# Performance work log

Hardware: AMD Instinct MI355X
Metric: run time of the kernel (lower is better)

Reference implementation:

```python
import jax, jax.numpy as jnp
import numpy as np

B, T, C, H, DFF = 4, 1024, 1024, 16, 4096
HS = C // H  # 64
EPS = 1e-5


def layer_norm(x, g, b):
    mu = jnp.mean(x, axis=-1, keepdims=True)
    var = jnp.var(x, axis=-1, keepdims=True)
    return (x - mu) * jax.lax.rsqrt(var + EPS) * g + b


def setup_inputs() -> dict:
    key = jax.random.key(0)
    ks = jax.random.split(key, 12)
    s = 0.02
    return {
        "x": jax.random.normal(ks[0], (B, T, C), jnp.float32),
        "wq": jax.random.normal(ks[1], (H, C, HS), jnp.float32) * s,
        "wk": jax.random.normal(ks[2], (H, C, HS), jnp.float32) * s,
        "wv": jax.random.normal(ks[3], (H, C, HS), jnp.float32) * s,
        "w_proj": jax.random.normal(ks[4], (H * HS, C), jnp.float32) * s,
        "b_proj": jnp.zeros((C,), jnp.float32),
        "w1": jax.random.normal(ks[5], (C, DFF), jnp.float32) * s,
        "b1": jnp.zeros((DFF,), jnp.float32),
        "w2": jax.random.normal(ks[6], (DFF, C), jnp.float32) * s,
        "b2": jnp.zeros((C,), jnp.float32),
        "g1": jnp.ones((C,), jnp.float32),
        "be1": jnp.zeros((C,), jnp.float32),
        "g2": jnp.ones((C,), jnp.float32),
        "be2": jnp.zeros((C,), jnp.float32),
    }


def reference(x, wq, wk, wv, w_proj, b_proj, w1, b1, w2, b2, g1, be1, g2, be2):
    h = layer_norm(x, g1, be1)
    # per-head projections, vectorized over heads: [B,H,T,HS]
    q = jnp.einsum('btc,hcd->bhtd', h, wq)
    k = jnp.einsum('btc,hcd->bhtd', h, wk)
    v = jnp.einsum('btc,hcd->bhtd', h, wv)
    # mask=None in the original forward, so no causal masking
    wei = jnp.einsum('bhtd,bhsd->bhts', q, k) * (HS ** -0.5)
    wei = jax.nn.softmax(wei, axis=-1)  # [B,H,T,T]
    out = jnp.einsum('bhts,bhsd->bhtd', wei, v)
    out = out.transpose(0, 2, 1, 3).reshape(B, T, H * HS)  # concat heads
    attn_out = out @ w_proj + b_proj
    x = x + attn_out
    h2 = layer_norm(x, g2, be2)
    ff = jax.nn.relu(h2 @ w1 + b1) @ w2 + b2
    x = x + ff
    return x, wei
```

## Files before the change

kernel.cpp:

```cpp
#include <hip/hip_runtime.h>
#include <hip/hip_bf16.h>

#define BB    4
#define TT    1024
#define CC    1024
#define HH    16
#define HSZ   64
#define DFF   4096
#define NTOK  (BB*TT)
#define BHN   (BB*HH)

typedef __attribute__((ext_vector_type(8))) short bf16x8;
typedef __attribute__((ext_vector_type(4))) float f32x4;

__device__ __forceinline__ ushort f2b(float v) {
    union { float f; unsigned u; } c; c.f = v;
    unsigned r = c.u + 0x7fffu + ((c.u >> 16) & 1u);
    return (ushort)(r >> 16);
}
__device__ __forceinline__ void stv(float* p, float v)  { *p = v; }
__device__ __forceinline__ void stv(ushort* p, float v) { *p = f2b(v); }

__device__ __forceinline__ void gload16(const void* g, void* l) {
    __builtin_amdgcn_global_load_lds(
        (const __attribute__((address_space(1))) void*)g,
        (__attribute__((address_space(3))) void*)l, 16, 0, 0);
}

__global__ __launch_bounds__(256)
void ln_k(const float* __restrict__ x, const float* __restrict__ g,
          const float* __restrict__ be, ushort* __restrict__ o)
{
    __shared__ float s1[4], s2[4];
    long row = blockIdx.x;
    const float4* xr = (const float4*)(x + row * CC);
    float4 v = xr[threadIdx.x];
    float a = v.x + v.y + v.z + v.w;
    float b = v.x*v.x + v.y*v.y + v.z*v.z + v.w*v.w;
    for (int off = 32; off > 0; off >>= 1) {
        a += __shfl_down(a, off);
        b += __shfl_down(b, off);
    }
    if ((threadIdx.x & 63) == 0) { s1[threadIdx.x >> 6] = a; s2[threadIdx.x >> 6] = b; }
    __syncthreads();
    float sum = s1[0] + s1[1] + s1[2] + s1[3];
    float sq  = s2[0] + s2[1] + s2[2] + s2[3];
    float mu  = sum * (1.0f / CC);
    float var = sq * (1.0f / CC) - mu * mu;
    float inv = rsqrtf(var + 1e-5f);
    float4 gg = ((const float4*)g)[threadIdx.x];
    float4 bb = ((const float4*)be)[threadIdx.x];
    ushort4 r;
    r.x = f2b((v.x - mu) * inv * gg.x + bb.x);
    r.y = f2b((v.y - mu) * inv * gg.y + bb.y);
    r.z = f2b((v.z - mu) * inv * gg.z + bb.z);
    r.w = f2b((v.w - mu) * inv * gg.w + bb.w);
    ((ushort4*)(o + row * CC))[threadIdx.x] = r;
}

__global__ __launch_bounds__(256)
void cvtall_k(const float* __restrict__ wq, const float* __restrict__ wk,
              const float* __restrict__ wv, const float* __restrict__ wproj,
              const float* __restrict__ w1, const float* __restrict__ w2,
              ushort* __restrict__ wqkvT, ushort* __restrict__ wpT,
              ushort* __restrict__ w1T, ushort* __restrict__ w2T)
{
    __shared__ float t[32][33];
    int idx = blockIdx.x;
    const float* src; ushort* dst; int R, Cc, bx, by;
    if (idx < 3072) {
        int seg = idx >> 10, rem = idx & 1023;
        int z = rem >> 6, tt2 = rem & 63;
        src = (seg == 0 ? wq : seg == 1 ? wk : wv) + (long)z * 65536;
        dst = wqkvT + (long)seg * (1L << 20) + (long)z * 65536;
        R = 1024; Cc = 64; bx = tt2 & 1; by = tt2 >> 1;
    } else if (idx < 4096) {
        int tt2 = idx - 3072;
        src = wproj; dst = wpT; R = 1024; Cc = 1024; bx = tt2 & 31; by = tt2 >> 5;
    } else if (idx < 8192) {
        int tt2 = idx - 4096;
        src = w1; dst = w1T; R = 1024; Cc = 4096; bx = tt2 & 127; by = tt2 >> 7;
    } else {
        int tt2 = idx - 8192;
        src = w2; dst = w2T; R = 4096; Cc = 1024; bx = tt2 & 31; by = tt2 >> 5;
    }
    int r0 = by * 32, c0 = bx * 32;
    int tx = threadIdx.x & 31, ty = threadIdx.x >> 5;
#pragma unroll
    for (int i = 0; i < 4; i++)
        t[ty + 8*i][tx] = src[(long)(r0 + ty + 8*i) * Cc + c0 + tx];
    __syncthreads();
#pragma unroll
    for (int i = 0; i < 4; i++)
        dst[(long)(c0 + ty + 8*i) * R + r0 + tx] = f2b(t[tx][ty + 8*i]);
}

enum { OL_PLAIN = 0, OL_QKV3 = 1 };
constexpr int EBIAS = 1, ERELU = 2, ERES = 4, ESCALE = 8;

template<int BM, int BN, int WM, int WN, int OL, int EPI, typename OutT>
__global__ __launch_bounds__(256)
void mgemm_k(const ushort* __restrict__ A, const ushort* __restrict__ Bt,
             const float* __restrict__ bias, const float* __restrict__ res,
             OutT* __restrict__ C, int M, int N, int K,
             long sA, long sB, long sC, float scale)
{
    constexpr int BK = 64;
    constexpr int FM = BM / WM / 16, FN = BN / WN / 16;
    __shared__ ushort As[BM * BK];
    __shared__ ushort Bs[BN * BK];
    const int tid = threadIdx.x;
    const int w = tid >> 6, l = tid & 63;
    const int wr = w / WN, wc = w % WN;
    const int l15 = l & 15, l4 = l >> 4;
    const int bh = blockIdx.z;
    const ushort* Ap = A  + (long)bh * sA + (long)(blockIdx.y * BM) * K;
    const ushort* Bp = Bt + (long)bh * sB + (long)(blockIdx.x * BN) * K;

    f32x4 acc[FM][FN];
#pragma unroll
    for (int m = 0; m < FM; m++)
#pragma unroll
        for (int n = 0; n < FN; n++) acc[m][n] = (f32x4){0.f, 0.f, 0.f, 0.f};

    const int arow = tid >> 3;
    const int achk = tid & 7;

    for (int k0 = 0; k0 < K; k0 += BK) {
#pragma unroll
        for (int i = 0; i < BM / 32; i++)
            gload16(Ap + (long)(i*32 + arow) * K + k0 + achk*8,
                    &As[(i*32 + w*8) * BK]);
#pragma unroll
        for (int i = 0; i < BN / 32; i++)
            gload16(Bp + (long)(i*32 + arow) * K + k0 + achk*8,
                    &Bs[(i*32 + w*8) * BK]);
        __syncthreads();
#pragma unroll
        for (int kk = 0; kk < 2; kk++) {
            const int ko = kk*32 + l4*8;
            bf16x8 af[FM], bfr[FN];
#pragma unroll
            for (int m = 0; m < FM; m++)
                af[m] = *(const bf16x8*)&As[(wr*(BM/WM) + m*16 + l15) * BK + ko];
#pragma unroll
            for (int n = 0; n < FN; n++)
                bfr[n] = *(const bf16x8*)&Bs[(wc*(BN/WN) + n*16 + l15) * BK + ko];
#pragma unroll
            for (int m = 0; m < FM; m++)
#pragma unroll
                for (int n = 0; n < FN; n++)
                    acc[m][n] = __builtin_amdgcn_mfma_f32_16x16x32_bf16(
                        af[m], bfr[n], acc[m][n], 0, 0, 0);
        }
        __syncthreads();
    }

#pragma unroll
    for (int m = 0; m < FM; m++) {
        int rbase = blockIdx.y*BM + wr*(BM/WM) + m*16 + l4*4;
#pragma unroll
        for (int n = 0; n < FN; n++) {
            int col = blockIdx.x*BN + wc*(BN/WN) + n*16 + l15;
#pragma unroll
            for (int r = 0; r < 4; r++) {
                int row = rbase + r;
                float v = acc[m][n][r];
                if (EPI & ESCALE) v *= scale;
                if (EPI & EBIAS)  v += bias[col];
                if (EPI & ERELU)  v = fmaxf(v, 0.f);
                if (EPI & ERES)   v += res[(long)row * N + col];
                long idx;
                if (OL == OL_PLAIN) {
                    idx = (long)row * N + col;
                } else {
                    int seg = col >> 10;
                    int cl  = col & 1023;
                    long bh_ = ((long)((row >> 10) * HH + (cl >> 6))) * 65536;
                    long off = (seg == 2)
                        ? bh_ + (long)(cl & 63) * 1024 + (row & 1023)
                        : bh_ + (long)(row & 1023) * 64 + (cl & 63);
                    idx = (long)seg * (4L << 20) + off;
                }
                stv(&C[(long)bh * sC + idx], v);
            }
        }
    }
}

__global__ __launch_bounds__(256, 2)
void fattn_k(const ushort* __restrict__ q_, const ushort* __restrict__ k_,
             const ushort* __restrict__ vt, float* __restrict__ wei,
             ushort* __restrict__ attn)
{
    __shared__ ushort Qs[128*64];
    __shared__ ushort Ks[128*64];
    __shared__ ushort Vs[64*128];
    __shared__ ushort Ps[128*128];
    float* sred = (float*)Ps;

    const int tid = threadIdx.x;
    const int w = tid >> 6, l = tid & 63;
    const int wr = w >> 1, wc = w & 1;
    const int l15 = l & 15, l4 = l >> 4;
    const int bh = blockIdx.y;
    const int q0 = blockIdx.x * 128;
    const int arow = tid >> 3, achk = tid & 7;
    const int kchk = achk ^ (arow & 7);
    const int vrow = tid >> 4;
    const int vchk = (tid & 15) ^ (vrow & 15);
    const int sw8  = (l15 & 7) << 3;
    const int sw16 = l15 << 3;

    const ushort* Qp = q_ + (long)bh * 65536;
    const ushort* Kp = k_ + (long)bh * 65536;
    const ushort* Vp = vt + (long)bh * 65536;

#pragma unroll
    for (int i = 0; i < 4; i++)
        gload16(Qp + (long)(q0 + i*32 + arow) * 64 + kchk*8, &Qs[(i*32 + w*8)*64]);

    float ssum[4][4];
#pragma unroll
    for (int m = 0; m < 4; m++)
#pragma unroll
        for (int r = 0; r < 4; r++) ssum[m][r] = 0.f;

    for (int st = 0; st < 8; ++st) {
#pragma unroll
        for (int i = 0; i < 4; i++)
            gload16(Kp + (long)(st*128 + i*32 + arow) * 64 + kchk*8,
                    &Ks[(i*32 + w*8)*64]);
        __syncthreads();

        f32x4 sacc[4][4];
#pragma unroll
        for (int m = 0; m < 4; m++)
#pragma unroll
            for (int n = 0; n < 4; n++) sacc[m][n] = (f32x4){0.f,0.f,0.f,0.f};
        __builtin_amdgcn_s_setprio(1);
#pragma unroll
        for (int kk = 0; kk < 2; kk++) {
            const int ko = kk*32 + l4*8;
            bf16x8 af[4], bfr[4];
#pragma unroll
            for (int m = 0; m < 4; m++)
                af[m] = *(const bf16x8*)&Qs[(wr*64 + m*16 + l15)*64 + (ko ^ sw8)];
#pragma unroll
            for (int n = 0; n < 4; n++)
                bfr[n] = *(const bf16x8*)&Ks[(wc*64 + n*16 + l15)*64 + (ko ^ sw8)];
#pragma unroll
            for (int m = 0; m < 4; m++)
#pragma unroll
                for (int n = 0; n < 4; n++)
                    sacc[m][n] = __builtin_amdgcn_mfma_f32_16x16x32_bf16(
                        af[m], bfr[n], sacc[m][n], 0, 0, 0);
        }
        __builtin_amdgcn_s_setprio(0);
#pragma unroll
        for (int m = 0; m < 4; m++)
#pragma unroll
            for (int r = 0; r < 4; r++) {
                float s = 0.f;
#pragma unroll
                for (int n = 0; n < 4; n++) s += __expf(sacc[m][n][r] * 0.125f);
                ssum[m][r] += s;
            }
        __syncthreads();
    }

    float linv[4][4];
#pragma unroll
    for (int m = 0; m < 4; m++)
#pragma unroll
        for (int r = 0; r < 4; r++) {
            float s = ssum[m][r];
#pragma unroll
            for (int d = 1; d < 16; d <<= 1) s += __shfl_xor(s, d);
            ssum[m][r] = s;
            if (l15 == 0) sred[wc*128 + wr*64 + m*16 + l4*4 + r] = s;
        }
    __syncthreads();
#pragma unroll
    for (int m = 0; m < 4; m++)
#pragma unroll
        for (int r = 0; r < 4; r++) {
            int rg = wr*64 + m*16 + l4*4 + r;
            linv[m][r] = 1.0f / (sred[rg] + sred[128 + rg]);
        }
    __syncthreads();

    f32x4 oacc[4][2];
#pragma unroll
    for (int m = 0; m < 4; m++)
#pragma unroll
        for (int n = 0; n < 2; n++) oacc[m][n] = (f32x4){0.f,0.f,0.f,0.f};

    for (int st = 0; st < 8; ++st) {
#pragma unroll
        for (int i = 0; i < 4; i++)
            gload16(Kp + (long)(st*128 + i*32 + arow) * 64 + kchk*8,
                    &Ks[(i*32 + w*8)*64]);
#pragma unroll
        for (int i = 0; i < 4; i++)
            gload16(Vp + (long)(i*16 + vrow) * 1024 + st*128 + vchk*8,
                    &Vs[(i*16 + w*4)*128]);
        __syncthreads();

        f32x4 sacc[4][4];
#pragma unroll
        for (int m = 0; m < 4; m++)
#pragma unroll
            for (int n = 0; n < 4; n++) sacc[m][n] = (f32x4){0.f,0.f,0.f,0.f};
        __builtin_amdgcn_s_setprio(1);
#pragma unroll
        for (int kk = 0; kk < 2; kk++) {
            const int ko = kk*32 + l4*8;
            bf16x8 af[4], bfr[4];
#pragma unroll
            for (int m = 0; m < 4; m++)
                af[m] = *(const bf16x8*)&Qs[(wr*64 + m*16 + l15)*64 + (ko ^ sw8)];
#pragma unroll
            for (int n = 0; n < 4; n++)
                bfr[n] = *(const bf16x8*)&Ks[(wc*64 + n*16 + l15)*64 + (ko ^ sw8)];
#pragma unroll
            for (int m = 0; m < 4; m++)
#pragma unroll
                for (int n = 0; n < 4; n++)
                    sacc[m][n] = __builtin_amdgcn_mfma_f32_16x16x32_bf16(
                        af[m], bfr[n], sacc[m][n], 0, 0, 0);
        }
        __builtin_amdgcn_s_setprio(0);

        float* wrow = wei + (long)bh * (TT*(long)TT) + st*128;
#pragma unroll
        for (int m = 0; m < 4; m++)
#pragma unroll
            for (int r = 0; r < 4; r++) {
                int rg = wr*64 + m*16 + l4*4 + r;
                int psw = (rg & 15) << 3;
                float li = linv[m][r];
#pragma unroll
                for (int n = 0; n < 4; n++) {
                    int col = wc*64 + n*16 + l15;
                    float p = __expf(sacc[m][n][r] * 0.125f) * li;
                    __builtin_nontemporal_store(p, &wrow[(long)(q0 + rg) * TT + col]);
                    Ps[rg*128 + (col ^ psw)] = f2b(p);
                }
            }
        __syncthreads();

        __builtin_amdgcn_s_setprio(1);
#pragma unroll
        for (int kc = 0; kc < 4; ++kc) {
            const int ko = kc*32 + l4*8;
            bf16x8 pa[4], vb[2];
#pragma unroll
            for (int m = 0; m < 4; m++)
                pa[m] = *(const bf16x8*)&Ps[(wr*64 + m*16 + l15)*128 + (ko ^ sw16)];
#pragma unroll
            for (int n = 0; n < 2; n++)
                vb[n] = *(const bf16x8*)&Vs[(wc*32 + n*16 + l15)*128 + (ko ^ sw16)];
#pragma unroll
            for (int m = 0; m < 4; m++)
#pragma unroll
                for (int n = 0; n < 2; n++)
                    oacc[m][n] = __builtin_amdgcn_mfma_f32_16x16x32_bf16(
                        pa[m], vb[n], oacc[m][n], 0, 0, 0);
        }
        __builtin_amdgcn_s_setprio(0);
        __syncthreads();
    }

#pragma unroll
    for (int m = 0; m < 4; m++)
#pragma unroll
        for (int r = 0; r < 4; r++) {
            int rg = wr*64 + m*16 + l4*4 + r;
            long rowbase = ((long)(bh >> 4) * TT + q0 + rg) * CC + (long)(bh & 15) * HSZ;
#pragma unroll
            for (int n = 0; n < 2; n++)
                attn[rowbase + wc*32 + n*16 + l15] = f2b(oacc[m][n][r]);
        }
}

extern "C" void kernel_launch(void* const* d_in, const int* in_sizes, int n_in,
                              void* d_out, int out_size, void* d_ws, size_t ws_size,
                              hipStream_t stream)
{
    const float* x      = (const float*)d_in[0];
    const float* wq     = (const float*)d_in[1];
    const float* wk     = (const float*)d_in[2];
    const float* wv     = (const float*)d_in[3];
    const float* w_proj = (const float*)d_in[4];
    const float* b_proj = (const float*)d_in[5];
    const float* w1     = (const float*)d_in[6];
    const float* b1     = (const float*)d_in[7];
    const float* w2     = (const float*)d_in[8];
    const float* b2     = (const float*)d_in[9];
    const float* g1     = (const float*)d_in[10];
    const float* be1    = (const float*)d_in[11];
    const float* g2     = (const float*)d_in[12];
    const float* be2    = (const float*)d_in[13];

    float* out_x = (float*)d_out;
    float* wei   = out_x + (long)NTOK * CC;

    const long MEL = 1 << 20;
    ushort* ws16 = (ushort*)d_ws;
    ushort* h    = ws16;
    ushort* q_   = ws16 + 4*MEL;
    ushort* k_   = ws16 + 8*MEL;
    ushort* vt   = ws16 + 12*MEL;
    ushort* attn = ws16 + 16*MEL;
    ushort* h2   = ws16 + 20*MEL;
    ushort* a1   = ws16 + 24*MEL;
    ushort* wqkvT= ws16 + 40*MEL;
    ushort* w1T  = ws16 + 44*MEL;
    ushort* wpT  = ws16 + 48*MEL;
    ushort* w2T  = ws16 + 49*MEL;
    float*  x1   = (float*)(ws16 + 54*MEL);

    cvtall_k<<<12288, 256, 0, stream>>>(wq, wk, wv, w_proj, w1, w2,
                                        wqkvT, wpT, w1T, w2T);

    ln_k<<<NTOK, 256, 0, stream>>>(x, g1, be1, h);

    mgemm_k<128,128,2,2,OL_QKV3,0,ushort><<<dim3(24,32,1), 256, 0, stream>>>(
        h, wqkvT, nullptr, nullptr, q_, NTOK, 3072, CC, 0,0,0, 0.f);

    fattn_k<<<dim3(8, 64), 256, 0, stream>>>(q_, k_, vt, wei, attn);

    mgemm_k<128,128,2,2,OL_PLAIN,EBIAS|ERES,float><<<dim3(8,32,1), 256, 0, stream>>>(
        attn, wpT, b_proj, x, x1, NTOK, CC, CC, 0,0,0, 0.f);

    ln_k<<<NTOK, 256, 0, stream>>>(x1, g2, be2, h2);

    mgemm_k<128,128,2,2,OL_PLAIN,EBIAS|ERELU,ushort><<<dim3(32,32,1), 256, 0, stream>>>(
        h2, w1T, b1, nullptr, a1, NTOK, DFF, CC, 0,0,0, 0.f);

    mgemm_k<128,128,2,2,OL_PLAIN,EBIAS|ERES,float><<<dim3(8,32,1), 256, 0, stream>>>(
        a1, w2T, b2, x1, out_x, NTOK, CC, DFF, 0,0,0, 0.f);
}
```

Before: 381.3 us.

## Double-buffer K tiles in softmax-sum pass and prefetch across attention phases

The first attention pass now ping-pongs K tiles between the Ks and Vs shared buffers, issuing the next tile's global-to-LDS load before computing on the current one and waiting with vmcnt(4) instead of a full sync. The first K/V tiles of the second pass are prefetched while the row-sum reduction runs. The wei stores are deferred until after the PV MFMAs so they do not sit in front of the barrier. Full __syncthreads are replaced with explicit waitcnt plus raw barriers, and one redundant barrier is removed. This adds register pressure (64 floats held for the deferred stores) and depends on hand-placed waitcnt counts being correct.

Result: faster. 369.4 us (-3.1%).

```diff
diff --git a/kernel.cpp b/kernel.cpp
--- a/kernel.cpp
+++ b/kernel.cpp
@@ -12,6 +12,13 @@
 
 typedef __attribute__((ext_vector_type(8))) short bf16x8;
 typedef __attribute__((ext_vector_type(4))) float f32x4;
+
+#define VMC0 asm volatile("s_waitcnt vmcnt(0)" ::: "memory")
+#define VMC4 asm volatile("s_waitcnt vmcnt(4)" ::: "memory")
+#define LGK0 asm volatile("s_waitcnt lgkmcnt(0)" ::: "memory")
+#define BARRIER do { asm volatile("" ::: "memory"); \
+                     __builtin_amdgcn_s_barrier();  \
+                     asm volatile("" ::: "memory"); } while (0)
 
 __device__ __forceinline__ ushort f2b(float v) {
     union { float f; unsigned u; } c; c.f = v;
@@ -219,6 +226,9 @@
 #pragma unroll
     for (int i = 0; i < 4; i++)
         gload16(Qp + (long)(q0 + i*32 + arow) * 64 + kchk*8, &Qs[(i*32 + w*8)*64]);
+#pragma unroll
+    for (int i = 0; i < 4; i++)
+        gload16(Kp + (long)(i*32 + arow) * 64 + kchk*8, &Ks[(i*32 + w*8)*64]);
 
     float ssum[4][4];
 #pragma unroll
@@ -227,11 +237,18 @@
         for (int r = 0; r < 4; r++) ssum[m][r] = 0.f;
 
     for (int st = 0; st < 8; ++st) {
-#pragma unroll
-        for (int i = 0; i < 4; i++)
-            gload16(Kp + (long)(st*128 + i*32 + arow) * 64 + kchk*8,
-                    &Ks[(i*32 + w*8)*64]);
-        __syncthreads();
+        const ushort* cur = (st & 1) ? Vs : Ks;
+        ushort*       nxt = (st & 1) ? Ks : Vs;
+        if (st < 7) {
+#pragma unroll
+            for (int i = 0; i < 4; i++)
+                gload16(Kp + (long)((st+1)*128 + i*32 + arow) * 64 + kchk*8,
+                        &nxt[(i*32 + w*8)*64]);
+            VMC4;
+        } else {
+            VMC0;
+        }
+        BARRIER;
 
         f32x4 sacc[4][4];
 #pragma unroll
@@ -248,7 +265,7 @@
                 af[m] = *(const bf16x8*)&Qs[(wr*64 + m*16 + l15)*64 + (ko ^ sw8)];
 #pragma unroll
             for (int n = 0; n < 4; n++)
-                bfr[n] = *(const bf16x8*)&Ks[(wc*64 + n*16 + l15)*64 + (ko ^ sw8)];
+                bfr[n] = *(const bf16x8*)&cur[(wc*64 + n*16 + l15)*64 + (ko ^ sw8)];
 #pragma unroll
             for (int m = 0; m < 4; m++)
 #pragma unroll
@@ -266,8 +283,15 @@
                 for (int n = 0; n < 4; n++) s += __expf(sacc[m][n][r] * 0.125f);
                 ssum[m][r] += s;
             }
-        __syncthreads();
-    }
+        BARRIER;
+    }
+
+#pragma unroll
+    for (int i = 0; i < 4; i++)
+        gload16(Kp + (long)(i*32 + arow) * 64 + kchk*8, &Ks[(i*32 + w*8)*64]);
+#pragma unroll
+    for (int i = 0; i < 4; i++)
+        gload16(Vp + (long)(i*16 + vrow) * 1024 + vchk*8, &Vs[(i*16 + w*4)*128]);
 
     float linv[4][4];
 #pragma unroll
@@ -277,10 +301,9 @@
             float s = ssum[m][r];
 #pragma unroll
             for (int d = 1; d < 16; d <<= 1) s += __shfl_xor(s, d);
-            ssum[m][r] = s;
             if (l15 == 0) sred[wc*128 + wr*64 + m*16 + l4*4 + r] = s;
         }
-    __syncthreads();
+    LGK0; BARRIER;
 #pragma unroll
     for (int m = 0; m < 4; m++)
 #pragma unroll
@@ -288,7 +311,6 @@
             int rg = wr*64 + m*16 + l4*4 + r;
             linv[m][r] = 1.0f / (sred[rg] + sred[128 + rg]);
         }
-    __syncthreads();
 
     f32x4 oacc[4][2];
 #pragma unroll
@@ -297,15 +319,18 @@
         for (int n = 0; n < 2; n++) oacc[m][n] = (f32x4){0.f,0.f,0.f,0.f};
 
     for (int st = 0; st < 8; ++st) {
-#pragma unroll
-        for (int i = 0; i < 4; i++)
-            gload16(Kp + (long)(st*128 + i*32 + arow) * 64 + kchk*8,
-                    &Ks[(i*32 + w*8)*64]);
-#pragma unroll
-        for (int i = 0; i < 4; i++)
-            gload16(Vp + (long)(i*16 + vrow) * 1024 + st*128 + vchk*8,
-                    &Vs[(i*16 + w*4)*128]);
-        __syncthreads();
+        if (st > 0) {
+#pragma unroll
+            for (int i = 0; i < 4; i++)
+                gload16(Kp + (long)(st*128 + i*32 + arow) * 64 + kchk*8,
+                        &Ks[(i*32 + w*8)*64]);
+#pragma unroll
+            for (int i = 0; i < 4; i++)
+                gload16(Vp + (long)(i*16 + vrow) * 1024 + st*128 + vchk*8,
+                        &Vs[(i*16 + w*4)*128]);
+        }
+        VMC0;
+        BARRIER;
 
         f32x4 sacc[4][4];
 #pragma unroll
@@ -332,7 +357,7 @@
         }
         __builtin_amdgcn_s_setprio(0);
 
-        float* wrow = wei + (long)bh * (TT*(long)TT) + st*128;
+        float pv[4][4][4];
 #pragma unroll
         for (int m = 0; m < 4; m++)
 #pragma unroll
@@ -344,11 +369,11 @@
                 for (int n = 0; n < 4; n++) {
                     int col = wc*64 + n*16 + l15;
                     float p = __expf(sacc[m][n][r] * 0.125f) * li;
-                    __builtin_nontemporal_store(p, &wrow[(long)(q0 + rg) * TT + col]);
+                    pv[m][n][r] = p;
                     Ps[rg*128 + (col ^ psw)] = f2b(p);
                 }
             }
-        __syncthreads();
+        LGK0; BARRIER;
 
         __builtin_amdgcn_s_setprio(1);
 #pragma unroll
@@ -369,7 +394,21 @@
                         pa[m], vb[n], oacc[m][n], 0, 0, 0);
         }
         __builtin_amdgcn_s_setprio(0);
-        __syncthreads();
+
+        float* wrow = wei + (long)bh * (TT*(long)TT) + st*128;
+#pragma unroll
+        for (int m = 0; m < 4; m++)
+#pragma unroll
+            for (int r = 0; r < 4; r++) {
+                int rg = wr*64 + m*16 + l4*4 + r;
+#pragma unroll
+                for (int n = 0; n < 4; n++) {
+                    int col = wc*64 + n*16 + l15;
+                    __builtin_nontemporal_store(pv[m][n][r],
+                        &wrow[(long)(q0 + rg) * TT + col]);
+                }
+            }
+        BARRIER;
     }
 
 #pragma unroll
```

## Restructure attention to per-wave query tiles reading K/V directly from global

Applied to the files above, without the earlier changes.

Rewrites the attention kernel so each wave owns 32 query rows, keeping Q fragments in registers and loading K and V^T fragments straight from global memory instead of staging them cooperatively in LDS. This removes nearly all block-level barriers, leaving only a small per-wave LDS buffer for P. The softmax scale and log2(e) are folded into Q in the QKV GEMM epilogue, so the kernel can use exp2f instead of a scaled expf. The grid is reordered so blocks of the same head run adjacently for L2 reuse of K/V, at the cost of redundant global/L2 traffic per wave and no LDS reuse of K/V across waves.

New measurement: 385.3 us. No clear change (+1.1%).

```diff
diff --git a/kernel.cpp b/kernel.cpp
--- a/kernel.cpp
+++ b/kernel.cpp
@@ -98,6 +98,8 @@
 enum { OL_PLAIN = 0, OL_QKV3 = 1 };
 constexpr int EBIAS = 1, ERELU = 2, ERES = 4, ESCALE = 8;
 
+#define QSCALE 0.18033688f
+
 template<int BM, int BN, int WM, int WN, int OL, int EPI, typename OutT>
 __global__ __launch_bounds__(256)
 void mgemm_k(const ushort* __restrict__ A, const ushort* __restrict__ Bt,
@@ -176,6 +178,7 @@
                 } else {
                     int seg = col >> 10;
                     int cl  = col & 1023;
+                    if (seg == 0) v *= QSCALE;
                     long bh_ = ((long)((row >> 10) * HH + (cl >> 6))) * 65536;
                     long off = (seg == 2)
                         ? bh_ + (long)(cl & 63) * 1024 + (row & 1023)
@@ -188,199 +191,152 @@
     }
 }
 
-__global__ __launch_bounds__(256, 2)
+__global__ __launch_bounds__(256)
 void fattn_k(const ushort* __restrict__ q_, const ushort* __restrict__ k_,
              const ushort* __restrict__ vt, float* __restrict__ wei,
              ushort* __restrict__ attn)
 {
-    __shared__ ushort Qs[128*64];
-    __shared__ ushort Ks[128*64];
-    __shared__ ushort Vs[64*128];
-    __shared__ ushort Ps[128*128];
-    float* sred = (float*)Ps;
+    __shared__ ushort Ps[4][32*64];
 
     const int tid = threadIdx.x;
-    const int w = tid >> 6, l = tid & 63;
-    const int wr = w >> 1, wc = w & 1;
+    const int wid = tid >> 6, l = tid & 63;
     const int l15 = l & 15, l4 = l >> 4;
-    const int bh = blockIdx.y;
-    const int q0 = blockIdx.x * 128;
-    const int arow = tid >> 3, achk = tid & 7;
-    const int kchk = achk ^ (arow & 7);
-    const int vrow = tid >> 4;
-    const int vchk = (tid & 15) ^ (vrow & 15);
-    const int sw8  = (l15 & 7) << 3;
-    const int sw16 = l15 << 3;
+    const int bh = blockIdx.x;
+    const int q0 = blockIdx.y * 128 + wid * 32;
+    const int sw = (l15 & 7) << 3;
 
     const ushort* Qp = q_ + (long)bh * 65536;
     const ushort* Kp = k_ + (long)bh * 65536;
     const ushort* Vp = vt + (long)bh * 65536;
-
-#pragma unroll
-    for (int i = 0; i < 4; i++)
-        gload16(Qp + (long)(q0 + i*32 + arow) * 64 + kchk*8, &Qs[(i*32 + w*8)*64]);
-
-    float ssum[4][4];
-#pragma unroll
-    for (int m = 0; m < 4; m++)
+    ushort* myPs = Ps[wid];
+
+    bf16x8 qf[2][2];
+#pragma unroll
+    for (int m = 0; m < 2; m++)
+#pragma unroll
+        for (int kk = 0; kk < 2; kk++)
+            qf[m][kk] = *(const bf16x8*)&Qp[(long)(q0 + m*16 + l15)*64 + kk*32 + l4*8];
+
+    float ssum[2][4];
+#pragma unroll
+    for (int m = 0; m < 2; m++)
 #pragma unroll
         for (int r = 0; r < 4; r++) ssum[m][r] = 0.f;
 
-    for (int st = 0; st < 8; ++st) {
-#pragma unroll
-        for (int i = 0; i < 4; i++)
-            gload16(Kp + (long)(st*128 + i*32 + arow) * 64 + kchk*8,
-                    &Ks[(i*32 + w*8)*64]);
-        __syncthreads();
-
-        f32x4 sacc[4][4];
-#pragma unroll
-        for (int m = 0; m < 4; m++)
+    for (int st = 0; st < 16; ++st) {
+        const ushort* Kt = Kp + (long)st * 64 * 64;
+        f32x4 sacc[2][4];
+#pragma unroll
+        for (int m = 0; m < 2; m++)
 #pragma unroll
             for (int n = 0; n < 4; n++) sacc[m][n] = (f32x4){0.f,0.f,0.f,0.f};
-        __builtin_amdgcn_s_setprio(1);
 #pragma unroll
         for (int kk = 0; kk < 2; kk++) {
-            const int ko = kk*32 + l4*8;
-            bf16x8 af[4], bfr[4];
-#pragma unroll
-            for (int m = 0; m < 4; m++)
-                af[m] = *(const bf16x8*)&Qs[(wr*64 + m*16 + l15)*64 + (ko ^ sw8)];
+            bf16x8 bfr[4];
 #pragma unroll
             for (int n = 0; n < 4; n++)
-                bfr[n] = *(const bf16x8*)&Ks[(wc*64 + n*16 + l15)*64 + (ko ^ sw8)];
-#pragma unroll
-            for (int m = 0; m < 4; m++)
+                bfr[n] = *(const bf16x8*)&Kt[(long)(n*16 + l15)*64 + kk*32 + l4*8];
+#pragma unroll
+            for (int m = 0; m < 2; m++)
 #pragma unroll
                 for (int n = 0; n < 4; n++)
                     sacc[m][n] = __builtin_amdgcn_mfma_f32_16x16x32_bf16(
-                        af[m], bfr[n], sacc[m][n], 0, 0, 0);
-        }
-        __builtin_amdgcn_s_setprio(0);
-#pragma unroll
-        for (int m = 0; m < 4; m++)
+                        qf[m][kk], bfr[n], sacc[m][n], 0, 0, 0);
+        }
+#pragma unroll
+        for (int m = 0; m < 2; m++)
 #pragma unroll
             for (int r = 0; r < 4; r++) {
                 float s = 0.f;
 #pragma unroll
-                for (int n = 0; n < 4; n++) s += __expf(sacc[m][n][r] * 0.125f);
+                for (int n = 0; n < 4; n++) s += exp2f(sacc[m][n][r]);
                 ssum[m][r] += s;
             }
-        __syncthreads();
-    }
-
-    float linv[4][4];
-#pragma unroll
-    for (int m = 0; m < 4; m++)
+    }
+
+    float linv[2][4];
+#pragma unroll
+    for (int m = 0; m < 2; m++)
 #pragma unroll
         for (int r = 0; r < 4; r++) {
             float s = ssum[m][r];
 #pragma unroll
             for (int d = 1; d < 16; d <<= 1) s += __shfl_xor(s, d);
-            ssum[m][r] = s;
-            if (l15 == 0) sred[wc*128 + wr*64 + m*16 + l4*4 + r] = s;
-        }
-    __syncthreads();
-#pragma unroll
-    for (int m = 0; m < 4; m++)
-#pragma unroll
-        for (int r = 0; r < 4; r++) {
-            int rg = wr*64 + m*16 + l4*4 + r;
-            linv[m][r] = 1.0f / (sred[rg] + sred[128 + rg]);
-        }
-    __syncthreads();
-
-    f32x4 oacc[4][2];
-#pragma unroll
-    for (int m = 0; m < 4; m++)
-#pragma unroll
-        for (int n = 0; n < 2; n++) oacc[m][n] = (f32x4){0.f,0.f,0.f,0.f};
-
-    for (int st = 0; st < 8; ++st) {
-#pragma unroll
-        for (int i = 0; i < 4; i++)
-            gload16(Kp + (long)(st*128 + i*32 + arow) * 64 + kchk*8,
-                    &Ks[(i*32 + w*8)*64]);
-#pragma unroll
-        for (int i = 0; i < 4; i++)
-            gload16(Vp + (long)(i*16 + vrow) * 1024 + st*128 + vchk*8,
-                    &Vs[(i*16 + w*4)*128]);
-        __syncthreads();
-
-        f32x4 sacc[4][4];
-#pragma unroll
-        for (int m = 0; m < 4; m++)
+            linv[m][r] = 1.0f / s;
+        }
+
+    f32x4 oacc[2][4];
+#pragma unroll
+    for (int m = 0; m < 2; m++)
+#pragma unroll
+        for (int n = 0; n < 4; n++) oacc[m][n] = (f32x4){0.f,0.f,0.f,0.f};
+
+    for (int st = 0; st < 16; ++st) {
+        const ushort* Kt = Kp + (long)st * 64 * 64;
+        f32x4 sacc[2][4];
+#pragma unroll
+        for (int m = 0; m < 2; m++)
 #pragma unroll
             for (int n = 0; n < 4; n++) sacc[m][n] = (f32x4){0.f,0.f,0.f,0.f};
-        __builtin_amdgcn_s_setprio(1);
 #pragma unroll
         for (int kk = 0; kk < 2; kk++) {
-            const int ko = kk*32 + l4*8;
-            bf16x8 af[4], bfr[4];
-#pragma unroll
-            for (int m = 0; m < 4; m++)
-                af[m] = *(const bf16x8*)&Qs[(wr*64 + m*16 + l15)*64 + (ko ^ sw8)];
+            bf16x8 bfr[4];
 #pragma unroll
             for (int n = 0; n < 4; n++)
-                bfr[n] = *(const bf16x8*)&Ks[(wc*64 + n*16 + l15)*64 + (ko ^ sw8)];
-#pragma unroll
-            for (int m = 0; m < 4; m++)
+                bfr[n] = *(const bf16x8*)&Kt[(long)(n*16 + l15)*64 + kk*32 + l4*8];
+#pragma unroll
+            for (int m = 0; m < 2; m++)
 #pragma unroll
                 for (int n = 0; n < 4; n++)
                     sacc[m][n] = __builtin_amdgcn_mfma_f32_16x16x32_bf16(
-                        af[m], bfr[n], sacc[m][n], 0, 0, 0);
-        }
-        __builtin_amdgcn_s_setprio(0);
-
-        float* wrow = wei + (long)bh * (TT*(long)TT) + st*128;
-#pragma unroll
-        for (int m = 0; m < 4; m++)
+                        qf[m][kk], bfr[n], sacc[m][n], 0, 0, 0);
+        }
+
+        float* wrow = wei + (long)bh * (TT*(long)TT) + st*64;
+#pragma unroll
+        for (int m = 0; m < 2; m++)
 #pragma unroll
             for (int r = 0; r < 4; r++) {
-                int rg = wr*64 + m*16 + l4*4 + r;
-                int psw = (rg & 15) << 3;
+                int lr = m*16 + l4*4 + r;
+                int psw = (lr & 7) << 3;
                 float li = linv[m][r];
 #pragma unroll
                 for (int n = 0; n < 4; n++) {
-                    int col = wc*64 + n*16 + l15;
-                    float p = __expf(sacc[m][n][r] * 0.125f) * li;
-                    __builtin_nontemporal_store(p, &wrow[(long)(q0 + rg) * TT + col]);
-                    Ps[rg*128 + (col ^ psw)] = f2b(p);
+                    int col = n*16 + l15;
+                    float p = exp2f(sacc[m][n][r]) * li;
+                    __builtin_nontemporal_store(p,
+                        &wrow[(long)(q0 + lr) * TT + col]);
+                    myPs[lr*64 + (col ^ psw)] = f2b(p);
                 }
             }
-        __syncthreads();
-
-        __builtin_amdgcn_s_setprio(1);
-#pragma unroll
-        for (int kc = 0; kc < 4; ++kc) {
-            const int ko = kc*32 + l4*8;
-            bf16x8 pa[4], vb[2];
-#pragma unroll
-            for (int m = 0; m < 4; m++)
-                pa[m] = *(const bf16x8*)&Ps[(wr*64 + m*16 + l15)*128 + (ko ^ sw16)];
-#pragma unroll
-            for (int n = 0; n < 2; n++)
-                vb[n] = *(const bf16x8*)&Vs[(wc*32 + n*16 + l15)*128 + (ko ^ sw16)];
-#pragma unroll
-            for (int m = 0; m < 4; m++)
-#pragma unroll
-                for (int n = 0; n < 2; n++)
+
+#pragma unroll
+        for (int kc = 0; kc < 2; ++kc) {
+            bf16x8 pa[2], vb[4];
+#pragma unroll
+            for (int m = 0; m < 2; m++)
+                pa[m] = *(const bf16x8*)&myPs[(m*16 + l15)*64 + ((kc*32 + l4*8) ^ sw)];
+#pragma unroll
+            for (int n = 0; n < 4; n++)
+                vb[n] = *(const bf16x8*)&Vp[(long)(n*16 + l15)*1024 + st*64 + kc*32 + l4*8];
+#pragma unroll
+            for (int m = 0; m < 2; m++)
+#pragma unroll
+                for (int n = 0; n < 4; n++)
                     oacc[m][n] = __builtin_amdgcn_mfma_f32_16x16x32_bf16(
                         pa[m], vb[n], oacc[m][n], 0, 0, 0);
         }
-        __builtin_amdgcn_s_setprio(0);
-        __syncthreads();
-    }
-
-#pragma unroll
-    for (int m = 0; m < 4; m++)
+    }
+
+#pragma unroll
+    for (int m = 0; m < 2; m++)
 #pragma unroll
         for (int r = 0; r < 4; r++) {
-            int rg = wr*64 + m*16 + l4*4 + r;
-            long rowbase = ((long)(bh >> 4) * TT + q0 + rg) * CC + (long)(bh & 15) * HSZ;
-#pragma unroll
-            for (int n = 0; n < 2; n++)
-                attn[rowbase + wc*32 + n*16 + l15] = f2b(oacc[m][n][r]);
+            int trow = q0 + m*16 + l4*4 + r;
+            long rowbase = ((long)(bh >> 4) * TT + trow) * CC + (long)(bh & 15) * HSZ;
+#pragma unroll
+            for (int n = 0; n < 4; n++)
+                attn[rowbase + n*16 + l15] = f2b(oacc[m][n][r]);
         }
 }
 
@@ -429,7 +385,7 @@
     mgemm_k<128,128,2,2,OL_QKV3,0,ushort><<<dim3(24,32,1), 256, 0, stream>>>(
         h, wqkvT, nullptr, nullptr, q_, NTOK, 3072, CC, 0,0,0, 0.f);
 
-    fattn_k<<<dim3(8, 64), 256, 0, stream>>>(q_, k_, vt, wei, attn);
+    fattn_k<<<dim3(64, 8), 256, 0, stream>>>(q_, k_, vt, wei, attn);
 
     mgemm_k<128,128,2,2,OL_PLAIN,EBIAS|ERES,float><<<dim3(8,32,1), 256, 0, stream>>>(
         attn, wpT, b_proj, x, x1, NTOK, CC, CC, 0,0,0, 0.f);
```
